# Optimization experiments

Hardware: AMD Instinct MI355X
Metric: run time of the kernel (lower is better)

The kernel has to match this reference:

```python
import jax, jax.numpy as jnp
import numpy as np

DIM = 128      # channels C
HEADS = 4
HD = DIM // HEADS  # head_dim = 32
N = 128        # window tokens = 2*8*8
BW = 2048      # B_ = batch * num_windows
NP = 256       # sp_mask partitions
NW = 256       # shift-mask windows
TABLE = 675    # (2*2-1)*(2*8-1)*(2*8-1)
SCALE = HD ** -0.5


def setup_inputs() -> dict:
    key = jax.random.key(0)
    ks = jax.random.split(key, 8)
    x = jax.random.normal(ks[0], (BW, N, DIM), jnp.float32)
    rpi = jax.random.randint(ks[1], (N, N), 0, TABLE, dtype=jnp.int32)
    mask = jax.random.normal(ks[2], (NW, N, N), jnp.float32)
    sp_mask = jax.random.normal(ks[3], (NP, N, N), jnp.float32)
    w_qkv = jax.random.normal(ks[4], (3 * DIM, DIM), jnp.float32) * 0.02
    b_qkv = jnp.zeros((3 * DIM,), jnp.float32)
    bias_table = jax.random.normal(ks[5], (TABLE, HEADS), jnp.float32) * 0.02
    w_proj = jax.random.normal(ks[6], (DIM, DIM), jnp.float32) * 0.02
    b_proj = jnp.zeros((DIM,), jnp.float32)
    return {"x": x, "rpi": rpi, "mask": mask, "sp_mask": sp_mask,
            "w_qkv": w_qkv, "b_qkv": b_qkv, "bias_table": bias_table,
            "w_proj": w_proj, "b_proj": b_proj}


def reference(x, rpi, mask, sp_mask, w_qkv, b_qkv, bias_table, w_proj, b_proj):
    B_, Nn, C = x.shape
    # qkv projection -> (B_, N, 3, H, hd)
    qkv = (x @ w_qkv.T + b_qkv).reshape(B_, Nn, 3, HEADS, HD)
    q = qkv[:, :, 0].transpose(0, 2, 1, 3) * SCALE  # (B_, H, N, hd)
    k = qkv[:, :, 1].transpose(0, 2, 1, 3)
    v = qkv[:, :, 2].transpose(0, 2, 1, 3)
    attn = jnp.einsum('bhnd,bhmd->bhnm', q, k)  # (B_, H, N, N)
    # gathered relative position bias: (N, N, H) -> (H, N, N)
    rpb = bias_table[rpi].transpose(2, 0, 1)
    attn = attn + rpb[None]
    # additive sparse mask, broadcast over B_//nP groups and heads
    attn = (attn.reshape(B_ // NP, NP, HEADS, Nn, Nn)
            + sp_mask[None, :, None]).reshape(B_, HEADS, Nn, Nn)
    # additive shift mask, broadcast over B_//nW groups and heads
    attn = (attn.reshape(B_ // NW, NW, HEADS, Nn, Nn)
            + mask[None, :, None]).reshape(B_, HEADS, Nn, Nn)
    attn = jax.nn.softmax(attn, axis=-1)
    out = jnp.einsum('bhnm,bhmd->bnhd', attn, v).reshape(B_, Nn, C)
    return out @ w_proj.T + b_proj
```

## Files before the change

kernel.cpp:

```cpp
#include <hip/hip_runtime.h>

typedef short v8s __attribute__((ext_vector_type(8)));
typedef float v4f __attribute__((ext_vector_type(4)));

#define MFMA16(a, b, c) __builtin_amdgcn_mfma_f32_16x16x32_bf16(a, b, c, 0, 0, 0)

__device__ __forceinline__ unsigned short f2b(float f) {
  union { float f; unsigned int i; } v;
  v.f = f;
  unsigned int x = v.i;
  return (unsigned short)((x + 0x7fffu + ((x >> 16) & 1u)) >> 16);
}
__device__ __forceinline__ v8s ld16u(const unsigned short* p) {
  union { v8s v; ushort4 h[2]; } u;
  u.h[0] = *(const ushort4*)(p);
  u.h[1] = *(const ushort4*)(p + 4);
  return u.v;
}
__device__ __forceinline__ void stage128(const float* __restrict__ src,
                                         unsigned short* __restrict__ xs, int tid) {
  for (int it = 0; it < 8; ++it) {
    int gl = tid + 256 * it;
    int row = gl >> 4, g = gl & 15;
    const float4* s = (const float4*)(src + row * 128 + g * 8);
    float4 a = s[0], b = s[1];
    union { int4 v; unsigned short u[8]; } pk;
    pk.u[0] = f2b(a.x); pk.u[1] = f2b(a.y); pk.u[2] = f2b(a.z); pk.u[3] = f2b(a.w);
    pk.u[4] = f2b(b.x); pk.u[5] = f2b(b.y); pk.u[6] = f2b(b.z); pk.u[7] = f2b(b.w);
    *(int4*)(xs + row * 128 + ((g ^ (row & 15)) << 3)) = pk.v;
  }
}

#define SCALE 0.17677669529663687f

#define WS_RPB 16777216
#define WS_WQH 17039360
#define WS_WPH 17137664

__global__ __launch_bounds__(256)
void conv_w(const float* __restrict__ wq, const float* __restrict__ wp,
            unsigned short* __restrict__ wqh, unsigned short* __restrict__ wph) {
  int i = blockIdx.x * 256 + threadIdx.x;
  if (i < 384 * 128) wqh[i] = f2b(wq[i]);
  else wph[i - 384 * 128] = f2b(wp[i - 384 * 128]);
}

__global__ __launch_bounds__(256)
void build_bias(const float* __restrict__ mask, const float* __restrict__ sp,
                const int* __restrict__ rpi, const float* __restrict__ btab,
                float* __restrict__ msumT, float* __restrict__ rpbT) {
  __shared__ float t[64][132];
  const int wgrp = blockIdx.x, tid = threadIdx.x;
  const float* mk = mask + (size_t)wgrp * 16384;
  const float* sk = sp + (size_t)wgrp * 16384;
  float* ot = msumT + (size_t)wgrp * 16384;
  for (int c = 0; c < 2; ++c) {
    for (int it = 0; it < 8; ++it) {
      int idx = tid + 256 * it;
      int nl = idx >> 5, f = idx & 31;
      float4 a = *(const float4*)(mk + (c * 64 + nl) * 128 + f * 4);
      float4 b = *(const float4*)(sk + (c * 64 + nl) * 128 + f * 4);
      float4 s;
      s.x = a.x + b.x; s.y = a.y + b.y; s.z = a.z + b.z; s.w = a.w + b.w;
      *(float4*)(&t[nl][f * 4]) = s;
    }
    __syncthreads();
    for (int it = 0; it < 8; ++it) {
      int idx = tid + 256 * it;
      int m = idx >> 4, j = idx & 15;
      float4 o;
      o.x = t[j * 4 + 0][m]; o.y = t[j * 4 + 1][m];
      o.z = t[j * 4 + 2][m]; o.w = t[j * 4 + 3][m];
      *(float4*)(ot + m * 128 + c * 64 + j * 4) = o;
    }
    __syncthreads();
  }
  int e = wgrp * 256 + tid;
  int rem = e & 16383;
  int h = e >> 14, m = rem >> 7, n = rem & 127;
  rpbT[e] = btab[rpi[n * 128 + m] * 4 + h];
}

__global__ __launch_bounds__(256, 3)
void attn_kernel(const float* __restrict__ xg,
                 const unsigned short* __restrict__ wqh,
                 const float* __restrict__ bq,
                 const float* __restrict__ msumT,
                 const float* __restrict__ rpbT,
                 float* __restrict__ o_ws) {
  __shared__ alignas(16) unsigned char smem[51456];
  unsigned short* ps  = (unsigned short*)smem;
  unsigned short* xs  = (unsigned short*)smem;
  unsigned short* kss = (unsigned short*)(smem + 33792);
  unsigned short* vs  = (unsigned short*)(smem + 43008);

  const int tid = threadIdx.x;
  const int wv = tid >> 6;
  const int lane = tid & 63;
  const int qd = lane >> 4;
  const int t16 = lane & 15;

  const int idx = blockIdx.x;
  const int wgrp = idx >> 5;
  const int rem = idx & 31;
  const int h = rem >> 3;
  const int b = (rem & 7) * 256 + wgrp;

  stage128(xg + (size_t)b * 16384, xs, tid);
  __syncthreads();

  v8s bx[2][4];
  for (int nt = 0; nt < 2; ++nt)
    for (int ks = 0; ks < 4; ++ks) {
      int n = 32 * wv + nt * 16 + t16;
      int g = ks * 4 + qd;
      bx[nt][ks] = *(const v8s*)(xs + n * 128 + ((g ^ (n & 15)) << 3));
    }

  v4f accqk[4][2];
  for (int jt = 0; jt < 4; ++jt)
    for (int nt = 0; nt < 2; ++nt) accqk[jt][nt] = v4f{0.f, 0.f, 0.f, 0.f};
  for (int jt = 0; jt < 4; ++jt) {
    int wbase = (jt < 2) ? (h * 32 + jt * 16) : (128 + h * 32 + (jt - 2) * 16);
    for (int ks = 0; ks < 4; ++ks) {
      v8s a = *(const v8s*)(wqh + (wbase + t16) * 128 + ks * 32 + 8 * qd);
      for (int nt = 0; nt < 2; ++nt)
        accqk[jt][nt] = MFMA16(a, bx[nt][ks], accqk[jt][nt]);
    }
  }
  v4f accv[2][2];
  for (int rt = 0; rt < 2; ++rt)
    for (int ct = 0; ct < 2; ++ct) accv[rt][ct] = v4f{0.f, 0.f, 0.f, 0.f};
  for (int ct = 0; ct < 2; ++ct)
    for (int ks = 0; ks < 4; ++ks) {
      v8s bw = *(const v8s*)(wqh + (256 + h * 32 + ct * 16 + t16) * 128 + ks * 32 + 8 * qd);
      for (int rt = 0; rt < 2; ++rt)
        accv[rt][ct] = MFMA16(bx[rt][ks], bw, accv[rt][ct]);
    }

  for (int jt = 2; jt < 4; ++jt)
    for (int nt = 0; nt < 2; ++nt) {
      int n = 32 * wv + nt * 16 + t16;
      ushort4 pk;
      float v0 = accqk[jt][nt][0] + bq[128 + h * 32 + (jt - 2) * 16 + 4 * qd + 0];
      float v1 = accqk[jt][nt][1] + bq[128 + h * 32 + (jt - 2) * 16 + 4 * qd + 1];
      float v2 = accqk[jt][nt][2] + bq[128 + h * 32 + (jt - 2) * 16 + 4 * qd + 2];
      float v3 = accqk[jt][nt][3] + bq[128 + h * 32 + (jt - 2) * 16 + 4 * qd + 3];
      pk.x = f2b(v0); pk.y = f2b(v1); pk.z = f2b(v2); pk.w = f2b(v3);
      *(ushort4*)(kss + n * 36 + (jt - 2) * 16 + 4 * qd) = pk;
    }
  for (int ct = 0; ct < 2; ++ct) {
    int d = ct * 16 + t16;
    float bv = bq[256 + h * 32 + d];
    for (int rt = 0; rt < 2; ++rt) {
      ushort4 pk;
      pk.x = f2b(accv[rt][ct][0] + bv);
      pk.y = f2b(accv[rt][ct][1] + bv);
      pk.z = f2b(accv[rt][ct][2] + bv);
      pk.w = f2b(accv[rt][ct][3] + bv);
      *(ushort4*)(vs + d * 132 + 32 * wv + rt * 16 + 4 * qd) = pk;
    }
  }

  unsigned int qpk[2][2][2];
  for (int jt = 0; jt < 2; ++jt)
    for (int nt = 0; nt < 2; ++nt) {
      float vv[4];
      for (int r = 0; r < 4; ++r)
        vv[r] = (accqk[jt][nt][r] + bq[h * 32 + jt * 16 + 4 * qd + r]) * SCALE;
      qpk[jt][nt][0] = (unsigned int)f2b(vv[0]) | ((unsigned int)f2b(vv[1]) << 16);
      qpk[jt][nt][1] = (unsigned int)f2b(vv[2]) | ((unsigned int)f2b(vv[3]) << 16);
    }
  const int srcA = ((qd & 1) << 5) + t16;
  const bool hiq = qd >= 2;
  v8s aq[2];
  for (int rt = 0; rt < 2; ++rt) {
    union { v8s v; unsigned int d[4]; } u;
    unsigned int a0 = __shfl((int)qpk[0][rt][0], srcA, 64);
    unsigned int b0 = __shfl((int)qpk[1][rt][0], srcA, 64);
    unsigned int a1 = __shfl((int)qpk[0][rt][1], srcA, 64);
    unsigned int b1 = __shfl((int)qpk[1][rt][1], srcA, 64);
    unsigned int a2 = __shfl((int)qpk[0][rt][0], srcA + 16, 64);
    unsigned int b2 = __shfl((int)qpk[1][rt][0], srcA + 16, 64);
    unsigned int a3 = __shfl((int)qpk[0][rt][1], srcA + 16, 64);
    unsigned int b3 = __shfl((int)qpk[1][rt][1], srcA + 16, 64);
    u.d[0] = hiq ? b0 : a0;
    u.d[1] = hiq ? b1 : a1;
    u.d[2] = hiq ? b2 : a2;
    u.d[3] = hiq ? b3 : a3;
    aq[rt] = u.v;
  }
  __syncthreads();

  v4f sa[2][8];
  const v4f zero4 = {0.f, 0.f, 0.f, 0.f};
  for (int ct = 0; ct < 8; ++ct) {
    int key = ct * 16 + t16;
    v8s bk = ld16u(kss + key * 36 + 8 * qd);
    for (int rt = 0; rt < 2; ++rt)
      sa[rt][ct] = MFMA16(aq[rt], bk, zero4);
  }
  {
    const float* mt = msumT + (size_t)wgrp * 16384;
    const float* rb = rpbT + (size_t)h * 16384;
    for (int ct = 0; ct < 8; ++ct) {
      int m = ct * 16 + t16;
      const float* pm = mt + m * 128;
      const float* pr = rb + m * 128;
      for (int rt = 0; rt < 2; ++rt) {
        int n0 = 32 * wv + rt * 16 + 4 * qd;
        float4 b1 = *(const float4*)(pm + n0);
        float4 b2 = *(const float4*)(pr + n0);
        sa[rt][ct][0] += b1.x + b2.x;
        sa[rt][ct][1] += b1.y + b2.y;
        sa[rt][ct][2] += b1.z + b2.z;
        sa[rt][ct][3] += b1.w + b2.w;
      }
    }
  }
  float pmax[2][4], pinv[2][4];
  for (int rt = 0; rt < 2; ++rt)
    for (int r = 0; r < 4; ++r) {
      float m0 = sa[rt][0][r];
      for (int ct = 1; ct < 8; ++ct) m0 = fmaxf(m0, sa[rt][ct][r]);
      m0 = fmaxf(m0, __shfl_xor(m0, 1));
      m0 = fmaxf(m0, __shfl_xor(m0, 2));
      m0 = fmaxf(m0, __shfl_xor(m0, 4));
      m0 = fmaxf(m0, __shfl_xor(m0, 8));
      pmax[rt][r] = m0;
    }
  for (int rt = 0; rt < 2; ++rt)
    for (int ct = 0; ct < 8; ++ct)
      for (int r = 0; r < 4; ++r)
        sa[rt][ct][r] = __expf(sa[rt][ct][r] - pmax[rt][r]);
  for (int rt = 0; rt < 2; ++rt)
    for (int r = 0; r < 4; ++r) {
      float s0 = 0.f;
      for (int ct = 0; ct < 8; ++ct) s0 += sa[rt][ct][r];
      s0 += __shfl_xor(s0, 1);
      s0 += __shfl_xor(s0, 2);
      s0 += __shfl_xor(s0, 4);
      s0 += __shfl_xor(s0, 8);
      pinv[rt][r] = 1.0f / s0;
    }
  for (int rt = 0; rt < 2; ++rt)
    for (int r = 0; r < 4; ++r) {
      int n = 32 * wv + rt * 16 + 4 * qd + r;
      for (int ct = 0; ct < 8; ++ct)
        ps[n * 132 + ct * 16 + t16] = f2b(sa[rt][ct][r] * pinv[rt][r]);
    }
  __syncthreads();

  v8s av[2][4];
  for (int rt = 0; rt < 2; ++rt)
    for (int ks = 0; ks < 4; ++ks) {
      int d = rt * 16 + t16;
      av[rt][ks] = ld16u(vs + d * 132 + ks * 32 + 8 * qd);
    }
  v4f oa[2][2];
  for (int rt = 0; rt < 2; ++rt)
    for (int ct = 0; ct < 2; ++ct) oa[rt][ct] = v4f{0.f, 0.f, 0.f, 0.f};
  for (int ct = 0; ct < 2; ++ct) {
    int n = 32 * wv + ct * 16 + t16;
    for (int ks = 0; ks < 4; ++ks) {
      v8s bp = ld16u(ps + n * 132 + ks * 32 + 8 * qd);
      for (int rt = 0; rt < 2; ++rt)
        oa[rt][ct] = MFMA16(av[rt][ks], bp, oa[rt][ct]);
    }
  }
  for (int rt = 0; rt < 2; ++rt)
    for (int ct = 0; ct < 2; ++ct) {
      int n = 32 * wv + ct * 16 + t16;
      int cbase = h * 32 + rt * 16 + 4 * qd;
      float4 pk;
      pk.x = oa[rt][ct][0];
      pk.y = oa[rt][ct][1];
      pk.z = oa[rt][ct][2];
      pk.w = oa[rt][ct][3];
      *(float4*)(o_ws + ((size_t)(b * 128 + n)) * 128 + cbase) = pk;
    }
}

__global__ __launch_bounds__(256, 3)
void proj_kernel(const unsigned short* __restrict__ wph,
                 const float* __restrict__ bpj,
                 float* __restrict__ out) {
  __shared__ alignas(16) unsigned short os[128 * 128];
  const int tid = threadIdx.x;
  const int wv = tid >> 6;
  const int lane = tid & 63;
  const int qd = lane >> 4;
  const int t16 = lane & 15;
  const size_t row0 = (size_t)blockIdx.x * 128;

  stage128(out + row0 * 128, os, tid);
  __syncthreads();

  v8s bo[2][4];
  for (int ct = 0; ct < 2; ++ct)
    for (int ks = 0; ks < 4; ++ks) {
      int n = 32 * wv + ct * 16 + t16;
      int g = ks * 4 + qd;
      bo[ct][ks] = *(const v8s*)(os + n * 128 + ((g ^ (n & 15)) << 3));
    }
  v4f acc[8][2];
  for (int rt = 0; rt < 8; ++rt)
    for (int ct = 0; ct < 2; ++ct) acc[rt][ct] = v4f{0.f, 0.f, 0.f, 0.f};
  for (int rt = 0; rt < 8; ++rt)
    for (int ks = 0; ks < 4; ++ks) {
      v8s a = *(const v8s*)(wph + (rt * 16 + t16) * 128 + ks * 32 + 8 * qd);
      for (int ct = 0; ct < 2; ++ct)
        acc[rt][ct] = MFMA16(a, bo[ct][ks], acc[rt][ct]);
    }
  for (int rt = 0; rt < 8; ++rt) {
    float4 bj = *(const float4*)(bpj + rt * 16 + 4 * qd);
    for (int ct = 0; ct < 2; ++ct) {
      int n = 32 * wv + ct * 16 + t16;
      float4 pk;
      pk.x = acc[rt][ct][0] + bj.x;
      pk.y = acc[rt][ct][1] + bj.y;
      pk.z = acc[rt][ct][2] + bj.z;
      pk.w = acc[rt][ct][3] + bj.w;
      *(float4*)(out + (row0 + n) * 128 + rt * 16 + 4 * qd) = pk;
    }
  }
}

extern "C" void kernel_launch(void* const* d_in, const int* in_sizes, int n_in,
                              void* d_out, int out_size, void* d_ws, size_t ws_size,
                              hipStream_t stream) {
  (void)in_sizes; (void)n_in; (void)out_size; (void)ws_size;
  const float* xg   = (const float*)d_in[0];
  const int*   rpi  = (const int*)d_in[1];
  const float* mask = (const float*)d_in[2];
  const float* sp   = (const float*)d_in[3];
  const float* wq   = (const float*)d_in[4];
  const float* bq   = (const float*)d_in[5];
  const float* btab = (const float*)d_in[6];
  const float* wp   = (const float*)d_in[7];
  const float* bpj  = (const float*)d_in[8];
  float* out = (float*)d_out;

  float* msumT = (float*)d_ws;
  float* rpbT  = (float*)((char*)d_ws + WS_RPB);
  unsigned short* wqh = (unsigned short*)((char*)d_ws + WS_WQH);
  unsigned short* wph = (unsigned short*)((char*)d_ws + WS_WPH);

  conv_w<<<256, 256, 0, stream>>>(wq, wp, wqh, wph);
  build_bias<<<256, 256, 0, stream>>>(mask, sp, rpi, btab, msumT, rpbT);
  attn_kernel<<<8192, 256, 0, stream>>>(xg, wqh, bq, msumT, rpbT, out);
  proj_kernel<<<2048, 256, 0, stream>>>(wph, bpj, out);
}
```

Before: 553.4 us.

## Keep softmax probabilities in registers and compute transposed scores to drop LDS staging

```diff
diff --git a/kernel.cpp b/kernel.cpp
--- a/kernel.cpp
+++ b/kernel.cpp
@@ -11,27 +11,24 @@
   unsigned int x = v.i;
   return (unsigned short)((x + 0x7fffu + ((x >> 16) & 1u)) >> 16);
 }
+__device__ __forceinline__ v8s ldf8(const float* p) {
+  float4 a = *(const float4*)p;
+  float4 b = *(const float4*)(p + 4);
+  union { v8s v; unsigned short u[8]; } r;
+  r.u[0] = f2b(a.x); r.u[1] = f2b(a.y); r.u[2] = f2b(a.z); r.u[3] = f2b(a.w);
+  r.u[4] = f2b(b.x); r.u[5] = f2b(b.y); r.u[6] = f2b(b.z); r.u[7] = f2b(b.w);
+  return r.v;
+}
 __device__ __forceinline__ v8s ld16u(const unsigned short* p) {
   union { v8s v; ushort4 h[2]; } u;
   u.h[0] = *(const ushort4*)(p);
   u.h[1] = *(const ushort4*)(p + 4);
   return u.v;
 }
-__device__ __forceinline__ void stage128(const float* __restrict__ src,
-                                         unsigned short* __restrict__ xs, int tid) {
-  for (int it = 0; it < 8; ++it) {
-    int gl = tid + 256 * it;
-    int row = gl >> 4, g = gl & 15;
-    const float4* s = (const float4*)(src + row * 128 + g * 8);
-    float4 a = s[0], b = s[1];
-    union { int4 v; unsigned short u[8]; } pk;
-    pk.u[0] = f2b(a.x); pk.u[1] = f2b(a.y); pk.u[2] = f2b(a.z); pk.u[3] = f2b(a.w);
-    pk.u[4] = f2b(b.x); pk.u[5] = f2b(b.y); pk.u[6] = f2b(b.z); pk.u[7] = f2b(b.w);
-    *(int4*)(xs + row * 128 + ((g ^ (row & 15)) << 3)) = pk.v;
-  }
-}
 
 #define SCALE 0.17677669529663687f
+#define LOG2E 1.4426950408889634f
+#define QSCALE (SCALE * LOG2E)
 
 #define WS_RPB 16777216
 #define WS_WQH 17039360
@@ -48,51 +45,35 @@
 __global__ __launch_bounds__(256)
 void build_bias(const float* __restrict__ mask, const float* __restrict__ sp,
                 const int* __restrict__ rpi, const float* __restrict__ btab,
-                float* __restrict__ msumT, float* __restrict__ rpbT) {
-  __shared__ float t[64][132];
+                float* __restrict__ msum, float* __restrict__ rpb) {
   const int wgrp = blockIdx.x, tid = threadIdx.x;
   const float* mk = mask + (size_t)wgrp * 16384;
   const float* sk = sp + (size_t)wgrp * 16384;
-  float* ot = msumT + (size_t)wgrp * 16384;
-  for (int c = 0; c < 2; ++c) {
-    for (int it = 0; it < 8; ++it) {
-      int idx = tid + 256 * it;
-      int nl = idx >> 5, f = idx & 31;
-      float4 a = *(const float4*)(mk + (c * 64 + nl) * 128 + f * 4);
-      float4 b = *(const float4*)(sk + (c * 64 + nl) * 128 + f * 4);
-      float4 s;
-      s.x = a.x + b.x; s.y = a.y + b.y; s.z = a.z + b.z; s.w = a.w + b.w;
-      *(float4*)(&t[nl][f * 4]) = s;
-    }
-    __syncthreads();
-    for (int it = 0; it < 8; ++it) {
-      int idx = tid + 256 * it;
-      int m = idx >> 4, j = idx & 15;
-      float4 o;
-      o.x = t[j * 4 + 0][m]; o.y = t[j * 4 + 1][m];
-      o.z = t[j * 4 + 2][m]; o.w = t[j * 4 + 3][m];
-      *(float4*)(ot + m * 128 + c * 64 + j * 4) = o;
-    }
-    __syncthreads();
+  float* ot = msum + (size_t)wgrp * 16384;
+  for (int it = 0; it < 16; ++it) {
+    int i = (tid + 256 * it) * 4;
+    float4 a = *(const float4*)(mk + i);
+    float4 b = *(const float4*)(sk + i);
+    float4 s;
+    s.x = (a.x + b.x) * LOG2E; s.y = (a.y + b.y) * LOG2E;
+    s.z = (a.z + b.z) * LOG2E; s.w = (a.w + b.w) * LOG2E;
+    *(float4*)(ot + i) = s;
   }
   int e = wgrp * 256 + tid;
-  int rem = e & 16383;
-  int h = e >> 14, m = rem >> 7, n = rem & 127;
-  rpbT[e] = btab[rpi[n * 128 + m] * 4 + h];
-}
-
-__global__ __launch_bounds__(256, 3)
+  int hh = e >> 14, r = e & 16383;
+  rpb[e] = btab[rpi[r] * 4 + hh] * LOG2E;
+}
+
+__global__ __launch_bounds__(256, 4)
 void attn_kernel(const float* __restrict__ xg,
                  const unsigned short* __restrict__ wqh,
                  const float* __restrict__ bq,
-                 const float* __restrict__ msumT,
-                 const float* __restrict__ rpbT,
+                 const float* __restrict__ msum,
+                 const float* __restrict__ rpb,
                  float* __restrict__ o_ws) {
-  __shared__ alignas(16) unsigned char smem[51456];
-  unsigned short* ps  = (unsigned short*)smem;
-  unsigned short* xs  = (unsigned short*)smem;
-  unsigned short* kss = (unsigned short*)(smem + 33792);
-  unsigned short* vs  = (unsigned short*)(smem + 43008);
+  __shared__ alignas(16) unsigned char smem[17664];
+  unsigned short* kss = (unsigned short*)smem;
+  unsigned short* vs  = (unsigned short*)(smem + 9216);
 
   const int tid = threadIdx.x;
   const int wv = tid >> 6;
@@ -106,15 +87,12 @@
   const int h = rem >> 3;
   const int b = (rem & 7) * 256 + wgrp;
 
-  stage128(xg + (size_t)b * 16384, xs, tid);
-  __syncthreads();
-
+  const float* xb = xg + (size_t)b * 16384;
   v8s bx[2][4];
   for (int nt = 0; nt < 2; ++nt)
     for (int ks = 0; ks < 4; ++ks) {
       int n = 32 * wv + nt * 16 + t16;
-      int g = ks * 4 + qd;
-      bx[nt][ks] = *(const v8s*)(xs + n * 128 + ((g ^ (n & 15)) << 3));
+      bx[nt][ks] = ldf8(xb + n * 128 + ks * 32 + 8 * qd);
     }
 
   v4f accqk[4][2];
@@ -167,7 +145,7 @@
     for (int nt = 0; nt < 2; ++nt) {
       float vv[4];
       for (int r = 0; r < 4; ++r)
-        vv[r] = (accqk[jt][nt][r] + bq[h * 32 + jt * 16 + 4 * qd + r]) * SCALE;
+        vv[r] = (accqk[jt][nt][r] + bq[h * 32 + jt * 16 + 4 * qd + r]) * QSCALE;
       qpk[jt][nt][0] = (unsigned int)f2b(vv[0]) | ((unsigned int)f2b(vv[1]) << 16);
       qpk[jt][nt][1] = (unsigned int)f2b(vv[2]) | ((unsigned int)f2b(vv[3]) << 16);
     }
@@ -195,113 +173,110 @@
   v4f sa[2][8];
   const v4f zero4 = {0.f, 0.f, 0.f, 0.f};
   for (int ct = 0; ct < 8; ++ct) {
-    int key = ct * 16 + t16;
-    v8s bk = ld16u(kss + key * 36 + 8 * qd);
-    for (int rt = 0; rt < 2; ++rt)
-      sa[rt][ct] = MFMA16(aq[rt], bk, zero4);
+    v8s bk = ld16u(kss + (ct * 16 + t16) * 36 + 8 * qd);
+    for (int nt = 0; nt < 2; ++nt)
+      sa[nt][ct] = MFMA16(bk, aq[nt], zero4);
   }
   {
-    const float* mt = msumT + (size_t)wgrp * 16384;
-    const float* rb = rpbT + (size_t)h * 16384;
-    for (int ct = 0; ct < 8; ++ct) {
-      int m = ct * 16 + t16;
-      const float* pm = mt + m * 128;
-      const float* pr = rb + m * 128;
-      for (int rt = 0; rt < 2; ++rt) {
-        int n0 = 32 * wv + rt * 16 + 4 * qd;
-        float4 b1 = *(const float4*)(pm + n0);
-        float4 b2 = *(const float4*)(pr + n0);
-        sa[rt][ct][0] += b1.x + b2.x;
-        sa[rt][ct][1] += b1.y + b2.y;
-        sa[rt][ct][2] += b1.z + b2.z;
-        sa[rt][ct][3] += b1.w + b2.w;
+    const float* mt = msum + (size_t)wgrp * 16384;
+    const float* rb = rpb + (size_t)h * 16384;
+    for (int nt = 0; nt < 2; ++nt) {
+      int n = 32 * wv + nt * 16 + t16;
+      const float* pm = mt + n * 128;
+      const float* pr = rb + n * 128;
+      for (int ct = 0; ct < 8; ++ct) {
+        float4 b1 = *(const float4*)(pm + ct * 16 + 4 * qd);
+        float4 b2 = *(const float4*)(pr + ct * 16 + 4 * qd);
+        sa[nt][ct][0] += b1.x + b2.x;
+        sa[nt][ct][1] += b1.y + b2.y;
+        sa[nt][ct][2] += b1.z + b2.z;
+        sa[nt][ct][3] += b1.w + b2.w;
       }
     }
   }
-  float pmax[2][4], pinv[2][4];
-  for (int rt = 0; rt < 2; ++rt)
-    for (int r = 0; r < 4; ++r) {
-      float m0 = sa[rt][0][r];
-      for (int ct = 1; ct < 8; ++ct) m0 = fmaxf(m0, sa[rt][ct][r]);
-      m0 = fmaxf(m0, __shfl_xor(m0, 1));
-      m0 = fmaxf(m0, __shfl_xor(m0, 2));
-      m0 = fmaxf(m0, __shfl_xor(m0, 4));
-      m0 = fmaxf(m0, __shfl_xor(m0, 8));
-      pmax[rt][r] = m0;
-    }
-  for (int rt = 0; rt < 2; ++rt)
+  float pinv[2];
+  for (int nt = 0; nt < 2; ++nt) {
+    float m0 = sa[nt][0][0];
+    for (int ct = 0; ct < 8; ++ct)
+      for (int r = 0; r < 4; ++r) m0 = fmaxf(m0, sa[nt][ct][r]);
+    m0 = fmaxf(m0, __shfl_xor(m0, 16));
+    m0 = fmaxf(m0, __shfl_xor(m0, 32));
     for (int ct = 0; ct < 8; ++ct)
       for (int r = 0; r < 4; ++r)
-        sa[rt][ct][r] = __expf(sa[rt][ct][r] - pmax[rt][r]);
-  for (int rt = 0; rt < 2; ++rt)
-    for (int r = 0; r < 4; ++r) {
-      float s0 = 0.f;
-      for (int ct = 0; ct < 8; ++ct) s0 += sa[rt][ct][r];
-      s0 += __shfl_xor(s0, 1);
-      s0 += __shfl_xor(s0, 2);
-      s0 += __shfl_xor(s0, 4);
-      s0 += __shfl_xor(s0, 8);
-      pinv[rt][r] = 1.0f / s0;
-    }
-  for (int rt = 0; rt < 2; ++rt)
-    for (int r = 0; r < 4; ++r) {
-      int n = 32 * wv + rt * 16 + 4 * qd + r;
-      for (int ct = 0; ct < 8; ++ct)
-        ps[n * 132 + ct * 16 + t16] = f2b(sa[rt][ct][r] * pinv[rt][r]);
-    }
-  __syncthreads();
+        sa[nt][ct][r] = exp2f(sa[nt][ct][r] - m0);
+    float s0 = 0.f;
+    for (int ct = 0; ct < 8; ++ct)
+      for (int r = 0; r < 4; ++r) s0 += sa[nt][ct][r];
+    s0 += __shfl_xor(s0, 16);
+    s0 += __shfl_xor(s0, 32);
+    pinv[nt] = 1.0f / s0;
+  }
 
   v8s av[2][4];
   for (int rt = 0; rt < 2; ++rt)
-    for (int ks = 0; ks < 4; ++ks) {
-      int d = rt * 16 + t16;
-      av[rt][ks] = ld16u(vs + d * 132 + ks * 32 + 8 * qd);
-    }
-  v4f oa[2][2];
-  for (int rt = 0; rt < 2; ++rt)
-    for (int ct = 0; ct < 2; ++ct) oa[rt][ct] = v4f{0.f, 0.f, 0.f, 0.f};
-  for (int ct = 0; ct < 2; ++ct) {
-    int n = 32 * wv + ct * 16 + t16;
-    for (int ks = 0; ks < 4; ++ks) {
-      v8s bp = ld16u(ps + n * 132 + ks * 32 + 8 * qd);
+    for (int ks = 0; ks < 4; ++ks)
+      av[rt][ks] = ld16u(vs + (rt * 16 + t16) * 132 + ks * 32 + 8 * qd);
+
+  const int srcP0 = ((qd & 1) << 5) + t16;
+  const bool hip2 = qd >= 2;
+  for (int nt = 0; nt < 2; ++nt) {
+    unsigned int pkd[8][2];
+    for (int ct = 0; ct < 8; ++ct) {
+      pkd[ct][0] = (unsigned int)f2b(sa[nt][ct][0]) | ((unsigned int)f2b(sa[nt][ct][1]) << 16);
+      pkd[ct][1] = (unsigned int)f2b(sa[nt][ct][2]) | ((unsigned int)f2b(sa[nt][ct][3]) << 16);
+    }
+    v8s bp[4];
+    for (int ks = 0; ks < 4; ++ks) {
+      union { v8s v; unsigned int d[4]; } u;
+      unsigned int a0 = __shfl((int)pkd[2 * ks][0], srcP0, 64);
+      unsigned int b0 = __shfl((int)pkd[2 * ks + 1][0], srcP0, 64);
+      unsigned int a1 = __shfl((int)pkd[2 * ks][1], srcP0, 64);
+      unsigned int b1 = __shfl((int)pkd[2 * ks + 1][1], srcP0, 64);
+      unsigned int a2 = __shfl((int)pkd[2 * ks][0], srcP0 + 16, 64);
+      unsigned int b2 = __shfl((int)pkd[2 * ks + 1][0], srcP0 + 16, 64);
+      unsigned int a3 = __shfl((int)pkd[2 * ks][1], srcP0 + 16, 64);
+      unsigned int b3 = __shfl((int)pkd[2 * ks + 1][1], srcP0 + 16, 64);
+      u.d[0] = hip2 ? b0 : a0;
+      u.d[1] = hip2 ? b1 : a1;
+      u.d[2] = hip2 ? b2 : a2;
+      u.d[3] = hip2 ? b3 : a3;
+      bp[ks] = u.v;
+    }
+    v4f oa[2] = {zero4, zero4};
+    for (int ks = 0; ks < 4; ++ks)
       for (int rt = 0; rt < 2; ++rt)
-        oa[rt][ct] = MFMA16(av[rt][ks], bp, oa[rt][ct]);
-    }
-  }
-  for (int rt = 0; rt < 2; ++rt)
-    for (int ct = 0; ct < 2; ++ct) {
-      int n = 32 * wv + ct * 16 + t16;
+        oa[rt] = MFMA16(av[rt][ks], bp[ks], oa[rt]);
+    int n = 32 * wv + nt * 16 + t16;
+    float s = pinv[nt];
+    for (int rt = 0; rt < 2; ++rt) {
       int cbase = h * 32 + rt * 16 + 4 * qd;
       float4 pk;
-      pk.x = oa[rt][ct][0];
-      pk.y = oa[rt][ct][1];
-      pk.z = oa[rt][ct][2];
-      pk.w = oa[rt][ct][3];
+      pk.x = oa[rt][0] * s;
+      pk.y = oa[rt][1] * s;
+      pk.z = oa[rt][2] * s;
+      pk.w = oa[rt][3] * s;
       *(float4*)(o_ws + ((size_t)(b * 128 + n)) * 128 + cbase) = pk;
     }
-}
-
-__global__ __launch_bounds__(256, 3)
+  }
+}
+
+__global__ __launch_bounds__(256, 4)
 void proj_kernel(const unsigned short* __restrict__ wph,
                  const float* __restrict__ bpj,
                  float* __restrict__ out) {
-  __shared__ alignas(16) unsigned short os[128 * 128];
   const int tid = threadIdx.x;
   const int wv = tid >> 6;
   const int lane = tid & 63;
   const int qd = lane >> 4;
   const int t16 = lane & 15;
   const size_t row0 = (size_t)blockIdx.x * 128;
-
-  stage128(out + row0 * 128, os, tid);
-  __syncthreads();
+  const float* src = out + row0 * 128;
 
   v8s bo[2][4];
   for (int ct = 0; ct < 2; ++ct)
     for (int ks = 0; ks < 4; ++ks) {
       int n = 32 * wv + ct * 16 + t16;
-      int g = ks * 4 + qd;
-      bo[ct][ks] = *(const v8s*)(os + n * 128 + ((g ^ (n & 15)) << 3));
+      bo[ct][ks] = ldf8(src + n * 128 + ks * 32 + 8 * qd);
     }
   v4f acc[8][2];
   for (int rt = 0; rt < 8; ++rt)
@@ -341,13 +316,13 @@
   const float* bpj  = (const float*)d_in[8];
   float* out = (float*)d_out;
 
-  float* msumT = (float*)d_ws;
-  float* rpbT  = (float*)((char*)d_ws + WS_RPB);
+  float* msum = (float*)d_ws;
+  float* rpb  = (float*)((char*)d_ws + WS_RPB);
   unsigned short* wqh = (unsigned short*)((char*)d_ws + WS_WQH);
   unsigned short* wph = (unsigned short*)((char*)d_ws + WS_WPH);
 
   conv_w<<<256, 256, 0, stream>>>(wq, wp, wqh, wph);
-  build_bias<<<256, 256, 0, stream>>>(mask, sp, rpi, btab, msumT, rpbT);
-  attn_kernel<<<8192, 256, 0, stream>>>(xg, wqh, bq, msumT, rpbT, out);
+  build_bias<<<256, 256, 0, stream>>>(mask, sp, rpi, btab, msum, rpb);
+  attn_kernel<<<8192, 256, 0, stream>>>(xg, wqh, bq, msum, rpb, out);
   proj_kernel<<<2048, 256, 0, stream>>>(wph, bpj, out);
 }
```

After: 553.0 us. No clear change (-0.1%).
